# Optimization experiments

Hardware: AMD Instinct MI355X
Metric: run time of the kernel (lower is better)

The kernel has to match this reference:

```python
import jax, jax.numpy as jnp
import numpy as np

N = 100000   # nodes
E = 800000   # edges (avg degree 8)
F = 64       # node feature dim
H = 64       # hidden units


def setup_inputs() -> dict:
    key = jax.random.key(0)
    ks = jax.random.split(key, 18)
    s = 0.05  # weight scale
    inp = {
        "node_feat": jax.random.normal(ks[0], (N, F), jnp.float32),
        "edge_weight": jax.random.uniform(ks[1], (E,), jnp.float32),
        "hidden_state": jax.random.normal(ks[2], (N, H), jnp.float32),
        "W_z": jax.random.normal(ks[3], (F, H), jnp.float32) * s,
        "b_z": jnp.zeros((H,), jnp.float32),
        "W_r": jax.random.normal(ks[4], (F, H), jnp.float32) * s,
        "b_r": jnp.zeros((H,), jnp.float32),
        "W_h": jax.random.normal(ks[5], (F, H), jnp.float32) * s,
        "b_h": jnp.zeros((H,), jnp.float32),
        "Wl_z": jax.random.normal(ks[6], (2 * H, H), jnp.float32) * s,
        "bl_z": jnp.zeros((H,), jnp.float32),
        "Wl_r": jax.random.normal(ks[7], (2 * H, H), jnp.float32) * s,
        "bl_r": jnp.zeros((H,), jnp.float32),
        "Wl_h": jax.random.normal(ks[8], (2 * H, H), jnp.float32) * s,
        "bl_h": jnp.zeros((H,), jnp.float32),
        "W_out": jax.random.normal(ks[9], (H, F), jnp.float32) * s,
        "b_out": jnp.zeros((F,), jnp.float32),
        "edge_index": jax.random.randint(ks[10], (2, E), 0, N, dtype=jnp.int64),
    }
    return inp


def _gcn(x, W, b, src, dst, w):
    # GCN-style graph conv with given (pre-normalized) edge weights:
    # out[v] = sum_{(u->v)} w_e * (x[u] @ W) + b
    m = x @ W                                   # [N, H] transform first (cheaper)
    msgs = m[src] * w[:, None]                  # [E, H] gather + scale
    return jax.ops.segment_sum(msgs, dst, num_segments=N) + b


def reference(node_feat, edge_weight, hidden_state,
              W_z, b_z, W_r, b_r, W_h, b_h,
              Wl_z, bl_z, Wl_r, bl_r, Wl_h, bl_h,
              W_out, b_out, edge_index):
    src, dst = edge_index[0], edge_index[1]
    # TGCN GRU gates
    cz = _gcn(node_feat, W_z, b_z, src, dst, edge_weight)          # [N, H]
    z = jax.nn.sigmoid(jnp.concatenate([cz, hidden_state], -1) @ Wl_z + bl_z)
    cr = _gcn(node_feat, W_r, b_r, src, dst, edge_weight)
    r = jax.nn.sigmoid(jnp.concatenate([cr, hidden_state], -1) @ Wl_r + bl_r)
    ch = _gcn(node_feat, W_h, b_h, src, dst, edge_weight)
    h_tilde = jnp.tanh(jnp.concatenate([ch, hidden_state * r], -1) @ Wl_h + bl_h)
    h = z * hidden_state + (1.0 - z) * h_tilde                     # [N, H]
    # readout
    y = jax.nn.relu(h) @ W_out + b_out                             # [N, F]
    return (y, h)
```

## Files before the change

kernel.cpp:

```cpp
#include <hip/hip_runtime.h>
#include <hip/hip_bf16.h>
#include <math.h>


typedef __attribute__((ext_vector_type(8))) short bf16x8;
typedef __attribute__((ext_vector_type(4))) float f32x4;

static __device__ __forceinline__ short f2bf(float x) {
    union { float f; unsigned u; } v; v.f = x;
    unsigned r = v.u + 0x7fffu + ((v.u >> 16) & 1u);
    return (short)(r >> 16);
}
__device__ __forceinline__ float sigmoid_(float x) { return 1.0f / (1.0f + __expf(-x)); }
__device__ __forceinline__ float tanh_(float x)    { return 1.0f - 2.0f / (__expf(2.0f * x) + 1.0f); }

__global__ __launch_bounds__(256) void prep_kernel(
    const float* __restrict__ x, short* __restrict__ xb,
    short* __restrict__ AXb, int n8)
{
    int i = blockIdx.x * blockDim.x + threadIdx.x;
    int stride = gridDim.x * blockDim.x;
    for (; i < n8; i += stride) {
        float4 a = ((const float4*)x)[i * 2];
        float4 b = ((const float4*)x)[i * 2 + 1];
        bf16x8 v;
        v[0] = f2bf(a.x); v[1] = f2bf(a.y); v[2] = f2bf(a.z); v[3] = f2bf(a.w);
        v[4] = f2bf(b.x); v[5] = f2bf(b.y); v[6] = f2bf(b.z); v[7] = f2bf(b.w);
        ((bf16x8*)xb)[i] = v;
        bf16x8 z = {0, 0, 0, 0, 0, 0, 0, 0};
        ((bf16x8*)AXb)[i] = z;
    }
}

__global__ __launch_bounds__(256) void fuse_weights_kernel(
    const float* __restrict__ Wz, const float* __restrict__ Wr, const float* __restrict__ Wh,
    const float* __restrict__ bz, const float* __restrict__ br, const float* __restrict__ bh,
    const float* __restrict__ Wlz, const float* __restrict__ Wlr, const float* __restrict__ Wlh,
    const float* __restrict__ blz, const float* __restrict__ blr, const float* __restrict__ blh,
    const float* __restrict__ Wout, const float* __restrict__ bout_,
    short* __restrict__ WT, float* __restrict__ bfv)
{
    int g = blockIdx.x;
    int tid = threadIdx.x;
    if (g == 3) {
        for (int i = tid; i < 4096; i += 256) {
            int k = i >> 6, n = i & 63;
            WT[6 * 4096 + n * 64 + k] = f2bf(Wout[k * 64 + n]);
        }
        if (tid < 64) bfv[192 + tid] = bout_[tid];
        return;
    }
    const float* Win = (g == 0) ? Wz : (g == 1) ? Wr : Wh;
    const float* Wl  = (g == 0) ? Wlz : (g == 1) ? Wlr : Wlh;
    const float* b   = (g == 0) ? bz : (g == 1) ? br : bh;
    const float* bl  = (g == 0) ? blz : (g == 1) ? blr : blh;

    __shared__ float wl_s[64][65];
    for (int i = tid; i < 4096; i += 256) wl_s[i >> 6][i & 63] = Wl[i];
    __syncthreads();

    int k = tid >> 2;
    int j0 = (tid & 3) << 4;
    float acc[16];
#pragma unroll
    for (int jj = 0; jj < 16; jj++) acc[jj] = 0.f;
    for (int t = 0; t < 64; t++) {
        float a = Win[k * 64 + t];
#pragma unroll
        for (int jj = 0; jj < 16; jj++) acc[jj] = fmaf(a, wl_s[t][j0 + jj], acc[jj]);
    }
#pragma unroll
    for (int jj = 0; jj < 16; jj++) WT[g * 4096 + (j0 + jj) * 64 + k] = f2bf(acc[jj]);

    for (int i = tid; i < 4096; i += 256) {
        int kk = i >> 6, n = i & 63;
        WT[(3 + g) * 4096 + n * 64 + kk] = f2bf(Wl[(64 + kk) * 64 + n]);
    }
    if (tid < 64) {
        float a2 = bl[tid];
        for (int t = 0; t < 64; t++) a2 = fmaf(b[t], wl_s[t][tid], a2);
        bfv[g * 64 + tid] = a2;
    }
}

__global__ __launch_bounds__(256) void scatter_kernel(
    const short* __restrict__ xb, const float* __restrict__ ew,
    const int* __restrict__ ei, short* __restrict__ AXb, int E)
{
    int hw  = (blockIdx.x * 256 + threadIdx.x) >> 5;
    int lj  = threadIdx.x & 31;
    int nhw = (gridDim.x * 256) >> 5;
    for (int e = hw; e < E; e += nhw) {
        int src = ei[e];
        int dst = ei[E + e];
        float w = ew[e];
        unsigned pv = *(const unsigned*)(xb + (size_t)src * 64 + lj * 2);
        float lo = __uint_as_float(pv << 16) * w;
        float hi = __uint_as_float(pv & 0xffff0000u) * w;
        unsigned pk = (unsigned)(unsigned short)f2bf(lo)
                    | ((unsigned)(unsigned short)f2bf(hi) << 16);
        short* addr = AXb + (size_t)dst * 64 + lj * 2;
        asm volatile("global_atomic_pk_add_bf16 %0, %1, off"
                     :: "v"(addr), "v"(pk) : "memory");
    }
    asm volatile("s_waitcnt vmcnt(0)" ::: "memory");
}

__global__ __launch_bounds__(256, 3) void gates_kernel(
    const short* __restrict__ AXb, const float* __restrict__ hid,
    const short* __restrict__ WT, const float* __restrict__ bfv,
    float* __restrict__ outY, float* __restrict__ outH, int nNodes)
{
    __shared__ short axs[64][72];
    __shared__ short hs [64][72];
    __shared__ short rsb[64][72];
    __shared__ float hf [64][68];

    const int tid  = threadIdx.x;
    const int w    = tid >> 6;
    const int lane = tid & 63;
    const int lr   = lane & 15;
    const int lg   = lane >> 4;
    const int col  = w * 16 + lr;
    const int n0   = blockIdx.x * 64;

    {
        int row = tid >> 2;
        int c0  = (tid & 3) << 4;
        int n   = n0 + row;
        bool valid = n < nNodes;
        const float4 z4 = make_float4(0.f, 0.f, 0.f, 0.f);
        const bf16x8 zb = {0, 0, 0, 0, 0, 0, 0, 0};
        bf16x8 a0 = valid ? *(const bf16x8*)(AXb + (size_t)n * 64 + c0)     : zb;
        bf16x8 a1 = valid ? *(const bf16x8*)(AXb + (size_t)n * 64 + c0 + 8) : zb;
        *(bf16x8*)(&axs[row][c0])     = a0;
        *(bf16x8*)(&axs[row][c0 + 8]) = a1;
#pragma unroll
        for (int q = 0; q < 4; q++) {
            float4 vh = valid ? *(const float4*)(hid + (size_t)n * 64 + c0 + q * 4) : z4;
            int c = c0 + q * 4;
            hs[row][c + 0] = f2bf(vh.x); hs[row][c + 1] = f2bf(vh.y);
            hs[row][c + 2] = f2bf(vh.z); hs[row][c + 3] = f2bf(vh.w);
            hf[row][c + 0] = vh.x; hf[row][c + 1] = vh.y;
            hf[row][c + 2] = vh.z; hf[row][c + 3] = vh.w;
        }
    }

    bf16x8 wf[7][2];
#pragma unroll
    for (int m = 0; m < 7; m++)
#pragma unroll
        for (int kb = 0; kb < 2; kb++)
            wf[m][kb] = *(const bf16x8*)(WT + m * 4096 + col * 64 + kb * 32 + lg * 8);
    const float bz_ = bfv[col], br_ = bfv[64 + col], bh_ = bfv[128 + col], bo_ = bfv[192 + col];

    __syncthreads();

    const f32x4 zero4 = {0.f, 0.f, 0.f, 0.f};
    f32x4 accz[4], accr[4], acch[4];
#pragma unroll
    for (int rt = 0; rt < 4; rt++) { accz[rt] = zero4; accr[rt] = zero4; acch[rt] = zero4; }

#pragma unroll
    for (int rt = 0; rt < 4; rt++) {
        int arow = rt * 16 + lr;
#pragma unroll
        for (int kb = 0; kb < 2; kb++) {
            bf16x8 aa = *(const bf16x8*)(&axs[arow][kb * 32 + lg * 8]);
            bf16x8 ah = *(const bf16x8*)(&hs [arow][kb * 32 + lg * 8]);
            accz[rt] = __builtin_amdgcn_mfma_f32_16x16x32_bf16(aa, wf[0][kb], accz[rt], 0, 0, 0);
            accr[rt] = __builtin_amdgcn_mfma_f32_16x16x32_bf16(aa, wf[1][kb], accr[rt], 0, 0, 0);
            acch[rt] = __builtin_amdgcn_mfma_f32_16x16x32_bf16(aa, wf[2][kb], acch[rt], 0, 0, 0);
            accz[rt] = __builtin_amdgcn_mfma_f32_16x16x32_bf16(ah, wf[3][kb], accz[rt], 0, 0, 0);
            accr[rt] = __builtin_amdgcn_mfma_f32_16x16x32_bf16(ah, wf[4][kb], accr[rt], 0, 0, 0);
        }
    }

    float zf[16];
#pragma unroll
    for (int rt = 0; rt < 4; rt++) {
#pragma unroll
        for (int i = 0; i < 4; i++) {
            int row = rt * 16 + lg * 4 + i;
            float z = sigmoid_(accz[rt][i] + bz_);
            float r = sigmoid_(accr[rt][i] + br_);
            zf[rt * 4 + i] = z;
            rsb[row][col] = f2bf(r * hf[row][col]);
        }
    }
    __syncthreads();

#pragma unroll
    for (int rt = 0; rt < 4; rt++) {
        int arow = rt * 16 + lr;
#pragma unroll
        for (int kb = 0; kb < 2; kb++) {
            bf16x8 ar = *(const bf16x8*)(&rsb[arow][kb * 32 + lg * 8]);
            acch[rt] = __builtin_amdgcn_mfma_f32_16x16x32_bf16(ar, wf[5][kb], acch[rt], 0, 0, 0);
        }
    }
#pragma unroll
    for (int rt = 0; rt < 4; rt++) {
#pragma unroll
        for (int i = 0; i < 4; i++) {
            int row = rt * 16 + lg * 4 + i;
            float ht = tanh_(acch[rt][i] + bh_);
            float z  = zf[rt * 4 + i];
            float hv = z * hf[row][col] + (1.f - z) * ht;
            int n = n0 + row;
            if (n < nNodes) outH[(size_t)n * 64 + col] = hv;
            axs[row][col] = f2bf(fmaxf(hv, 0.f));
        }
    }
    __syncthreads();

    f32x4 accy[4];
#pragma unroll
    for (int rt = 0; rt < 4; rt++) accy[rt] = zero4;
#pragma unroll
    for (int rt = 0; rt < 4; rt++) {
        int arow = rt * 16 + lr;
#pragma unroll
        for (int kb = 0; kb < 2; kb++) {
            bf16x8 aa = *(const bf16x8*)(&axs[arow][kb * 32 + lg * 8]);
            accy[rt] = __builtin_amdgcn_mfma_f32_16x16x32_bf16(aa, wf[6][kb], accy[rt], 0, 0, 0);
        }
    }
#pragma unroll
    for (int rt = 0; rt < 4; rt++) {
#pragma unroll
        for (int i = 0; i < 4; i++) {
            int row = rt * 16 + lg * 4 + i;
            int n = n0 + row;
            if (n < nNodes) outY[(size_t)n * 64 + col] = accy[rt][i] + bo_;
        }
    }
}

extern "C" void kernel_launch(void* const* d_in, const int* in_sizes, int n_in,
                              void* d_out, int out_size, void* d_ws, size_t ws_size,
                              hipStream_t stream)
{
    const float* node_feat = (const float*)d_in[0];
    const float* edge_w    = (const float*)d_in[1];
    const float* hidden    = (const float*)d_in[2];
    const float* W_z  = (const float*)d_in[3];
    const float* b_z  = (const float*)d_in[4];
    const float* W_r  = (const float*)d_in[5];
    const float* b_r  = (const float*)d_in[6];
    const float* W_h  = (const float*)d_in[7];
    const float* b_h  = (const float*)d_in[8];
    const float* Wl_z = (const float*)d_in[9];
    const float* bl_z = (const float*)d_in[10];
    const float* Wl_r = (const float*)d_in[11];
    const float* bl_r = (const float*)d_in[12];
    const float* Wl_h = (const float*)d_in[13];
    const float* bl_h = (const float*)d_in[14];
    const float* W_out = (const float*)d_in[15];
    const float* b_out = (const float*)d_in[16];
    const int*   edge_index = (const int*)d_in[17];

    const int N = in_sizes[0] / 64;
    const int E = in_sizes[1];

    short* AXb = (short*)d_ws;
    short* xb  = AXb + (size_t)N * 64;
    short* WT  = xb + (size_t)N * 64;
    float* bfv = (float*)(WT + 7 * 4096);

    float* outY = (float*)d_out;
    float* outH = outY + (size_t)N * 64;

    prep_kernel<<<2048, 256, 0, stream>>>(node_feat, xb, AXb, N * 8);
    fuse_weights_kernel<<<4, 256, 0, stream>>>(W_z, W_r, W_h, b_z, b_r, b_h,
                                               Wl_z, Wl_r, Wl_h, bl_z, bl_r, bl_h,
                                               W_out, b_out, WT, bfv);
    scatter_kernel<<<2048, 256, 0, stream>>>(xb, edge_w, edge_index, AXb, E);

    int nblk = (N + 63) / 64;
    gates_kernel<<<nblk, 256, 0, stream>>>(AXb, hidden, WT, bfv, outY, outH, N);
}
```

Baseline: 151.7 us.

## Replace atomic edge scatter with per-destination ELL bucket build and gather aggregation

Edges are bucketed by destination into a fixed-width ELL table, up to 16 slots per node, using one int atomic per edge. A gather kernel then sums the neighbour features per node in fp32, with no per-feature atomics. Edges that overflow the 16 slots fall back to bf16 packed atomics. This removes the heavy bf16 atomic traffic and the separate bf16 conversion of x. In exchange it adds an extra kernel, workspace for the ELL table and counts, and random fp32 gathers of x. It uses the ELL path only when the workspace is large enough and otherwise keeps the old path.

```diff
diff --git a/kernel.cpp b/kernel.cpp
--- a/kernel.cpp
+++ b/kernel.cpp
@@ -2,6 +2,8 @@
 #include <hip/hip_bf16.h>
 #include <math.h>
 
+
+#define PAD 16
 
 typedef __attribute__((ext_vector_type(8))) short bf16x8;
 typedef __attribute__((ext_vector_type(4))) float f32x4;
@@ -14,13 +16,85 @@
 __device__ __forceinline__ float sigmoid_(float x) { return 1.0f / (1.0f + __expf(-x)); }
 __device__ __forceinline__ float tanh_(float x)    { return 1.0f - 2.0f / (__expf(2.0f * x) + 1.0f); }
 
+__global__ __launch_bounds__(256) void prep_ell_kernel(
+    short* __restrict__ AXb, int* __restrict__ cnt, int N)
+{
+    int gid = blockIdx.x * blockDim.x + threadIdx.x;
+    int stride = gridDim.x * blockDim.x;
+    for (int i = gid; i < N; i += stride) cnt[i] = 0;
+    const uint4 z = make_uint4(0, 0, 0, 0);
+    int n16 = N * 8;
+    for (int i = gid; i < n16; i += stride) ((uint4*)AXb)[i] = z;
+}
+
+__global__ __launch_bounds__(256) void build_ell_kernel(
+    const int* __restrict__ ei, const float* __restrict__ ew,
+    const float* __restrict__ x, int* __restrict__ cnt,
+    uint2* __restrict__ ELL, short* __restrict__ AXb, int E)
+{
+    int i = blockIdx.x * 256 + threadIdx.x;
+    if (i < E) {
+        int src = ei[i];
+        int dst = ei[E + i];
+        float w = ew[i];
+        int rank = atomicAdd(&cnt[dst], 1);
+        if (rank < PAD) {
+            ELL[(size_t)dst * PAD + rank] = make_uint2((unsigned)src, __float_as_uint(w));
+        } else {
+#pragma unroll 4
+            for (int j = 0; j < 32; j++) {
+                float2 xv = *(const float2*)(x + (size_t)src * 64 + j * 2);
+                unsigned pk = (unsigned)(unsigned short)f2bf(xv.x * w)
+                            | ((unsigned)(unsigned short)f2bf(xv.y * w) << 16);
+                short* addr = AXb + (size_t)dst * 64 + j * 2;
+                asm volatile("global_atomic_pk_add_bf16 %0, %1, off"
+                             :: "v"(addr), "v"(pk) : "memory");
+            }
+        }
+    }
+    asm volatile("s_waitcnt vmcnt(0)" ::: "memory");
+}
+
+__global__ __launch_bounds__(512) void aggregate_ell_kernel(
+    const float* __restrict__ x, const uint2* __restrict__ ELL,
+    const int* __restrict__ cnt, short* __restrict__ AXb, int N)
+{
+    int hw = (blockIdx.x * 512 + threadIdx.x) >> 5;
+    int lj = threadIdx.x & 31;
+    if (hw >= N) return;
+    int deg = min(cnt[hw], PAD);
+    const uint2* row = ELL + (size_t)hw * PAD;
+    float a0 = 0.f, a1 = 0.f;
+    int e = 0;
+    for (; e + 1 < deg; e += 2) {
+        uint2 m0 = row[e], m1 = row[e + 1];
+        float2 x0 = *(const float2*)(x + (size_t)m0.x * 64 + lj * 2);
+        float2 x1 = *(const float2*)(x + (size_t)m1.x * 64 + lj * 2);
+        float w0 = __uint_as_float(m0.y), w1 = __uint_as_float(m1.y);
+        a0 = fmaf(x0.x, w0, a0); a1 = fmaf(x0.y, w0, a1);
+        a0 = fmaf(x1.x, w1, a0); a1 = fmaf(x1.y, w1, a1);
+    }
+    if (e < deg) {
+        uint2 m = row[e];
+        float2 xv = *(const float2*)(x + (size_t)m.x * 64 + lj * 2);
+        float w = __uint_as_float(m.y);
+        a0 = fmaf(xv.x, w, a0); a1 = fmaf(xv.y, w, a1);
+    }
+    unsigned prev = *(unsigned*)(AXb + (size_t)hw * 64 + lj * 2);
+    a0 += __uint_as_float(prev << 16);
+    a1 += __uint_as_float(prev & 0xffff0000u);
+    unsigned pk = (unsigned)(unsigned short)f2bf(a0)
+                | ((unsigned)(unsigned short)f2bf(a1) << 16);
+    *(unsigned*)(AXb + (size_t)hw * 64 + lj * 2) = pk;
+}
+
 __global__ __launch_bounds__(256) void prep_kernel(
     const float* __restrict__ x, short* __restrict__ xb,
     short* __restrict__ AXb, int n8)
 {
-    int i = blockIdx.x * blockDim.x + threadIdx.x;
+    int gid = blockIdx.x * blockDim.x + threadIdx.x;
     int stride = gridDim.x * blockDim.x;
-    for (; i < n8; i += stride) {
+    for (int i = gid; i < n8; i += stride) {
         float4 a = ((const float4*)x)[i * 2];
         float4 b = ((const float4*)x)[i * 2 + 1];
         bf16x8 v;
@@ -29,57 +103,6 @@
         ((bf16x8*)xb)[i] = v;
         bf16x8 z = {0, 0, 0, 0, 0, 0, 0, 0};
         ((bf16x8*)AXb)[i] = z;
-    }
-}
-
-__global__ __launch_bounds__(256) void fuse_weights_kernel(
-    const float* __restrict__ Wz, const float* __restrict__ Wr, const float* __restrict__ Wh,
-    const float* __restrict__ bz, const float* __restrict__ br, const float* __restrict__ bh,
-    const float* __restrict__ Wlz, const float* __restrict__ Wlr, const float* __restrict__ Wlh,
-    const float* __restrict__ blz, const float* __restrict__ blr, const float* __restrict__ blh,
-    const float* __restrict__ Wout, const float* __restrict__ bout_,
-    short* __restrict__ WT, float* __restrict__ bfv)
-{
-    int g = blockIdx.x;
-    int tid = threadIdx.x;
-    if (g == 3) {
-        for (int i = tid; i < 4096; i += 256) {
-            int k = i >> 6, n = i & 63;
-            WT[6 * 4096 + n * 64 + k] = f2bf(Wout[k * 64 + n]);
-        }
-        if (tid < 64) bfv[192 + tid] = bout_[tid];
-        return;
-    }
-    const float* Win = (g == 0) ? Wz : (g == 1) ? Wr : Wh;
-    const float* Wl  = (g == 0) ? Wlz : (g == 1) ? Wlr : Wlh;
-    const float* b   = (g == 0) ? bz : (g == 1) ? br : bh;
-    const float* bl  = (g == 0) ? blz : (g == 1) ? blr : blh;
-
-    __shared__ float wl_s[64][65];
-    for (int i = tid; i < 4096; i += 256) wl_s[i >> 6][i & 63] = Wl[i];
-    __syncthreads();
-
-    int k = tid >> 2;
-    int j0 = (tid & 3) << 4;
-    float acc[16];
-#pragma unroll
-    for (int jj = 0; jj < 16; jj++) acc[jj] = 0.f;
-    for (int t = 0; t < 64; t++) {
-        float a = Win[k * 64 + t];
-#pragma unroll
-        for (int jj = 0; jj < 16; jj++) acc[jj] = fmaf(a, wl_s[t][j0 + jj], acc[jj]);
-    }
-#pragma unroll
-    for (int jj = 0; jj < 16; jj++) WT[g * 4096 + (j0 + jj) * 64 + k] = f2bf(acc[jj]);
-
-    for (int i = tid; i < 4096; i += 256) {
-        int kk = i >> 6, n = i & 63;
-        WT[(3 + g) * 4096 + n * 64 + kk] = f2bf(Wl[(64 + kk) * 64 + n]);
-    }
-    if (tid < 64) {
-        float a2 = bl[tid];
-        for (int t = 0; t < 64; t++) a2 = fmaf(b[t], wl_s[t][tid], a2);
-        bfv[g * 64 + tid] = a2;
     }
 }
 
@@ -104,6 +127,57 @@
                      :: "v"(addr), "v"(pk) : "memory");
     }
     asm volatile("s_waitcnt vmcnt(0)" ::: "memory");
+}
+
+__global__ __launch_bounds__(256) void fuse_weights_kernel(
+    const float* __restrict__ Wz, const float* __restrict__ Wr, const float* __restrict__ Wh,
+    const float* __restrict__ bz, const float* __restrict__ br, const float* __restrict__ bh,
+    const float* __restrict__ Wlz, const float* __restrict__ Wlr, const float* __restrict__ Wlh,
+    const float* __restrict__ blz, const float* __restrict__ blr, const float* __restrict__ blh,
+    const float* __restrict__ Wout, const float* __restrict__ bout_,
+    short* __restrict__ WT, float* __restrict__ bfv)
+{
+    int g = blockIdx.x;
+    int tid = threadIdx.x;
+    if (g == 3) {
+        for (int i = tid; i < 4096; i += 256) {
+            int k = i >> 6, n = i & 63;
+            WT[6 * 4096 + n * 64 + k] = f2bf(Wout[k * 64 + n]);
+        }
+        if (tid < 64) bfv[192 + tid] = bout_[tid];
+        return;
+    }
+    const float* Win = (g == 0) ? Wz : (g == 1) ? Wr : Wh;
+    const float* Wl  = (g == 0) ? Wlz : (g == 1) ? Wlr : Wlh;
+    const float* b   = (g == 0) ? bz : (g == 1) ? br : bh;
+    const float* bl  = (g == 0) ? blz : (g == 1) ? blr : blh;
+
+    __shared__ float wl_s[64][65];
+    for (int i = tid; i < 4096; i += 256) wl_s[i >> 6][i & 63] = Wl[i];
+    __syncthreads();
+
+    int k = tid >> 2;
+    int j0 = (tid & 3) << 4;
+    float acc[16];
+#pragma unroll
+    for (int jj = 0; jj < 16; jj++) acc[jj] = 0.f;
+    for (int t = 0; t < 64; t++) {
+        float a = Win[k * 64 + t];
+#pragma unroll
+        for (int jj = 0; jj < 16; jj++) acc[jj] = fmaf(a, wl_s[t][j0 + jj], acc[jj]);
+    }
+#pragma unroll
+    for (int jj = 0; jj < 16; jj++) WT[g * 4096 + (j0 + jj) * 64 + k] = f2bf(acc[jj]);
+
+    for (int i = tid; i < 4096; i += 256) {
+        int kk = i >> 6, n = i & 63;
+        WT[(3 + g) * 4096 + n * 64 + kk] = f2bf(Wl[(64 + kk) * 64 + n]);
+    }
+    if (tid < 64) {
+        float a2 = bl[tid];
+        for (int t = 0; t < 64; t++) a2 = fmaf(b[t], wl_s[t][tid], a2);
+        bfv[g * 64 + tid] = a2;
+    }
 }
 
 __global__ __launch_bounds__(256, 3) void gates_kernel(
@@ -263,19 +337,34 @@
     const int N = in_sizes[0] / 64;
     const int E = in_sizes[1];
 
-    short* AXb = (short*)d_ws;
-    short* xb  = AXb + (size_t)N * 64;
-    short* WT  = xb + (size_t)N * 64;
-    float* bfv = (float*)(WT + 7 * 4096);
+    char* ws = (char*)d_ws;
+    size_t off = 0;
+    short* AXb = (short*)(ws + off); off += (size_t)N * 64 * 2;
+    char*  uni = ws + off;           off += (size_t)N * PAD * 8;
+    short* WT  = (short*)(ws + off); off += 7 * 4096 * 2;
+    float* bfv = (float*)(ws + off); off += 4 * 64 * 4;
+    int*   cnt = (int*)(ws + off);   off += (size_t)N * 4;
+
+    const bool useELL = (ws_size >= off) && (N <= (1 << 20));
 
     float* outY = (float*)d_out;
     float* outH = outY + (size_t)N * 64;
 
-    prep_kernel<<<2048, 256, 0, stream>>>(node_feat, xb, AXb, N * 8);
     fuse_weights_kernel<<<4, 256, 0, stream>>>(W_z, W_r, W_h, b_z, b_r, b_h,
                                                Wl_z, Wl_r, Wl_h, bl_z, bl_r, bl_h,
                                                W_out, b_out, WT, bfv);
-    scatter_kernel<<<2048, 256, 0, stream>>>(xb, edge_w, edge_index, AXb, E);
+    if (useELL) {
+        uint2* ELL = (uint2*)uni;
+        prep_ell_kernel<<<2048, 256, 0, stream>>>(AXb, cnt, N);
+        build_ell_kernel<<<(E + 255) / 256, 256, 0, stream>>>(
+            edge_index, edge_w, node_feat, cnt, ELL, AXb, E);
+        aggregate_ell_kernel<<<(N * 32 + 511) / 512, 512, 0, stream>>>(
+            node_feat, ELL, cnt, AXb, N);
+    } else {
+        short* xb = (short*)uni;
+        prep_kernel<<<2048, 256, 0, stream>>>(node_feat, xb, AXb, N * 8);
+        scatter_kernel<<<2048, 256, 0, stream>>>(xb, edge_w, edge_index, AXb, E);
+    }
 
     int nblk = (N + 63) / 64;
     gates_kernel<<<nblk, 256, 0, stream>>>(AXb, hidden, WT, bfv, outY, outH, N);
```

After: 168.7 us. +11.2%, slower.

## Drop bf16 feature copy, gather fp32 directly, and trim gates LDS usage

Applied to the files above, without the earlier changes.

The prep kernel no longer converts node features to bf16 and now only zeroes the aggregation buffer, while the scatter kernel reads fp32 features straight from the input. The scatter and zero kernels switch from grid-stride loops to one edge or chunk per thread-group. The gates kernel drops its fp32 hidden-state LDS copy, reuses the bf16 copy for the blend, and removes the launch-bounds occupancy hint. This saves a full pass over the features and some shared memory. In exchange the scatter gathers twice as many bytes per edge, and the hidden state in the final blend is rounded to bf16.

```diff
diff --git a/kernel.cpp b/kernel.cpp
--- a/kernel.cpp
+++ b/kernel.cpp
@@ -11,25 +11,18 @@
     unsigned r = v.u + 0x7fffu + ((v.u >> 16) & 1u);
     return (short)(r >> 16);
 }
+static __device__ __forceinline__ float bf2f(short s) {
+    return __uint_as_float((unsigned)(unsigned short)s << 16);
+}
 __device__ __forceinline__ float sigmoid_(float x) { return 1.0f / (1.0f + __expf(-x)); }
 __device__ __forceinline__ float tanh_(float x)    { return 1.0f - 2.0f / (__expf(2.0f * x) + 1.0f); }
 
-__global__ __launch_bounds__(256) void prep_kernel(
-    const float* __restrict__ x, short* __restrict__ xb,
-    short* __restrict__ AXb, int n8)
-{
-    int i = blockIdx.x * blockDim.x + threadIdx.x;
-    int stride = gridDim.x * blockDim.x;
-    for (; i < n8; i += stride) {
-        float4 a = ((const float4*)x)[i * 2];
-        float4 b = ((const float4*)x)[i * 2 + 1];
-        bf16x8 v;
-        v[0] = f2bf(a.x); v[1] = f2bf(a.y); v[2] = f2bf(a.z); v[3] = f2bf(a.w);
-        v[4] = f2bf(b.x); v[5] = f2bf(b.y); v[6] = f2bf(b.z); v[7] = f2bf(b.w);
-        ((bf16x8*)xb)[i] = v;
-        bf16x8 z = {0, 0, 0, 0, 0, 0, 0, 0};
-        ((bf16x8*)AXb)[i] = z;
-    }
+__global__ __launch_bounds__(256) void prep_zero_kernel(
+    short* __restrict__ AXb, int n16)
+{
+    int i = blockIdx.x * 256 + threadIdx.x;
+    const uint4 z = make_uint4(0, 0, 0, 0);
+    if (i < n16) ((uint4*)AXb)[i] = z;
 }
 
 __global__ __launch_bounds__(256) void fuse_weights_kernel(
@@ -84,21 +77,18 @@
 }
 
 __global__ __launch_bounds__(256) void scatter_kernel(
-    const short* __restrict__ xb, const float* __restrict__ ew,
+    const float* __restrict__ x, const float* __restrict__ ew,
     const int* __restrict__ ei, short* __restrict__ AXb, int E)
 {
-    int hw  = (blockIdx.x * 256 + threadIdx.x) >> 5;
-    int lj  = threadIdx.x & 31;
-    int nhw = (gridDim.x * 256) >> 5;
-    for (int e = hw; e < E; e += nhw) {
+    int e  = (blockIdx.x * 256 + threadIdx.x) >> 5;
+    int lj = threadIdx.x & 31;
+    if (e < E) {
         int src = ei[e];
         int dst = ei[E + e];
         float w = ew[e];
-        unsigned pv = *(const unsigned*)(xb + (size_t)src * 64 + lj * 2);
-        float lo = __uint_as_float(pv << 16) * w;
-        float hi = __uint_as_float(pv & 0xffff0000u) * w;
-        unsigned pk = (unsigned)(unsigned short)f2bf(lo)
-                    | ((unsigned)(unsigned short)f2bf(hi) << 16);
+        float2 xv = *(const float2*)(x + (size_t)src * 64 + lj * 2);
+        unsigned pk = (unsigned)(unsigned short)f2bf(xv.x * w)
+                    | ((unsigned)(unsigned short)f2bf(xv.y * w) << 16);
         short* addr = AXb + (size_t)dst * 64 + lj * 2;
         asm volatile("global_atomic_pk_add_bf16 %0, %1, off"
                      :: "v"(addr), "v"(pk) : "memory");
@@ -106,7 +96,7 @@
     asm volatile("s_waitcnt vmcnt(0)" ::: "memory");
 }
 
-__global__ __launch_bounds__(256, 3) void gates_kernel(
+__global__ __launch_bounds__(256) void gates_kernel(
     const short* __restrict__ AXb, const float* __restrict__ hid,
     const short* __restrict__ WT, const float* __restrict__ bfv,
     float* __restrict__ outY, float* __restrict__ outH, int nNodes)
@@ -114,7 +104,6 @@
     __shared__ short axs[64][72];
     __shared__ short hs [64][72];
     __shared__ short rsb[64][72];
-    __shared__ float hf [64][68];
 
     const int tid  = threadIdx.x;
     const int w    = tid >> 6;
@@ -141,8 +130,6 @@
             int c = c0 + q * 4;
             hs[row][c + 0] = f2bf(vh.x); hs[row][c + 1] = f2bf(vh.y);
             hs[row][c + 2] = f2bf(vh.z); hs[row][c + 3] = f2bf(vh.w);
-            hf[row][c + 0] = vh.x; hf[row][c + 1] = vh.y;
-            hf[row][c + 2] = vh.z; hf[row][c + 3] = vh.w;
         }
     }
 
@@ -185,7 +172,7 @@
             float z = sigmoid_(accz[rt][i] + bz_);
             float r = sigmoid_(accr[rt][i] + br_);
             zf[rt * 4 + i] = z;
-            rsb[row][col] = f2bf(r * hf[row][col]);
+            rsb[row][col] = f2bf(r * bf2f(hs[row][col]));
         }
     }
     __syncthreads();
@@ -206,7 +193,7 @@
             int row = rt * 16 + lg * 4 + i;
             float ht = tanh_(acch[rt][i] + bh_);
             float z  = zf[rt * 4 + i];
-            float hv = z * hf[row][col] + (1.f - z) * ht;
+            float hv = z * bf2f(hs[row][col]) + (1.f - z) * ht;
             int n = n0 + row;
             if (n < nNodes) outH[(size_t)n * 64 + col] = hv;
             axs[row][col] = f2bf(fmaxf(hv, 0.f));
@@ -263,19 +250,21 @@
     const int N = in_sizes[0] / 64;
     const int E = in_sizes[1];
 
-    short* AXb = (short*)d_ws;
-    short* xb  = AXb + (size_t)N * 64;
-    short* WT  = xb + (size_t)N * 64;
-    float* bfv = (float*)(WT + 7 * 4096);
+    char* ws = (char*)d_ws;
+    size_t off = 0;
+    short* AXb = (short*)(ws + off); off += (size_t)N * 64 * 2;
+    short* WT  = (short*)(ws + off); off += 7 * 4096 * 2;
+    float* bfv = (float*)(ws + off); off += 4 * 64 * 4;
 
     float* outY = (float*)d_out;
     float* outH = outY + (size_t)N * 64;
 
-    prep_kernel<<<2048, 256, 0, stream>>>(node_feat, xb, AXb, N * 8);
+    prep_zero_kernel<<<(N * 8 + 255) / 256, 256, 0, stream>>>(AXb, N * 8);
     fuse_weights_kernel<<<4, 256, 0, stream>>>(W_z, W_r, W_h, b_z, b_r, b_h,
                                                Wl_z, Wl_r, Wl_h, bl_z, bl_r, bl_h,
                                                W_out, b_out, WT, bfv);
-    scatter_kernel<<<2048, 256, 0, stream>>>(xb, edge_w, edge_index, AXb, E);
+    scatter_kernel<<<(E * 32 + 255) / 256, 256, 0, stream>>>(
+        node_feat, edge_w, edge_index, AXb, E);
 
     int nblk = (N + 63) / 64;
     gates_kernel<<<nblk, 256, 0, stream>>>(AXb, hidden, WT, bfv, outY, outH, N);
```

Measured after the change: 152.4 us. No clear change (+0.4%).
